# Optimization experiments

Hardware: AMD Instinct MI355X
Metric: run time of the kernel (lower is better)

Reference implementation:

```python
import jax, jax.numpy as jnp
import numpy as np

H = 16  # hidden_size
I = 30  # GRU input_size (hard-coded in module)


def setup_inputs() -> dict:
    key = jax.random.key(0)
    ks = jax.random.split(key, 12)
    B, T = 4096, 512
    s = lambda k, sh: jax.random.normal(k, sh, jnp.float32) * 0.1
    return {
        "x": jax.random.normal(ks[0], (B, T, I), jnp.float32),
        "lengths": jax.random.randint(ks[1], (B,), 1, T + 1),  # valid lengths in [1, T]
        "w_ih": s(ks[2], (3 * H, I)),
        "w_hh": s(ks[3], (3 * H, H)),
        "b_ih": s(ks[4], (3 * H,)),
        "b_hh": s(ks[5], (3 * H,)),
        "fc1_w": s(ks[6], (H, H)), "fc1_b": s(ks[7], (H,)),
        "fc2_w": s(ks[8], (H, H)), "fc2_b": s(ks[9], (H,)),
        "fc3_w": s(ks[10], (H, H)), "fc3_b": s(ks[11], (H,)),
    }


def _gru_last_hidden(x, lengths, w_ih, w_hh, b_ih, b_hh):
    """Run GRU over padded [B,T,I] and return hidden at t = lengths-1 per row.
    Equivalent to pack_padded -> GRU -> pad_packed -> gather output[b, len-1],
    since h_t only depends on steps <= t."""
    B, T, _ = x.shape
    # Precompute input-side gate activations for all steps: [B,T,3H]
    xg = jnp.einsum('bti,gi->btg', x, w_ih) + b_ih
    xr, xz, xn = jnp.split(xg, 3, axis=-1)
    w_hr, w_hz, w_hn = jnp.split(w_hh, 3, axis=0)
    b_hr, b_hz, b_hn = jnp.split(b_hh, 3)
    tidx = lengths - 1  # [B]

    def step(carry, inp):
        h, last = carry
        t, xr_t, xz_t, xn_t = inp
        r = jax.nn.sigmoid(xr_t + h @ w_hr.T + b_hr)
        z = jax.nn.sigmoid(xz_t + h @ w_hz.T + b_hz)
        n = jnp.tanh(xn_t + r * (h @ w_hn.T + b_hn))
        h = (1.0 - z) * n + z * h
        last = jnp.where((tidx == t)[:, None], h, last)  # capture h at final valid step
        return (h, last), None

    h0 = jnp.zeros((B, H), x.dtype)
    (_, last), _ = jax.lax.scan(
        step, (h0, h0),
        (jnp.arange(T),
         xr.transpose(1, 0, 2), xz.transpose(1, 0, 2), xn.transpose(1, 0, 2)))
    return last  # [B,H]


def reference(x, lengths, w_ih, w_hh, b_ih, b_hh,
              fc1_w, fc1_b, fc2_w, fc2_b, fc3_w, fc3_b):
    h = _gru_last_hidden(x, lengths, w_ih, w_hh, b_ih, b_hh)
    e = h @ fc1_w.T + fc1_b
    e = jax.nn.relu(e) @ fc2_w.T + fc2_b   # dropout is identity in eval mode
    e = jax.nn.relu(e) @ fc3_w.T + fc3_b
    return e
```

## Files before the change

kernel.cpp:

```cpp
#include <hip/hip_runtime.h>
#include <cstdint>
#include <cstddef>

typedef float v2f __attribute__((ext_vector_type(2)));

#define HID 16
#define IN  30

#define FAST_RCP(x) __builtin_amdgcn_rcpf(x)

__device__ __forceinline__ float bperm(int baddr, float v) {
    return __int_as_float(__builtin_amdgcn_ds_bpermute(baddr, __float_as_int(v)));
}
__device__ __forceinline__ float dppswap1(float v) {
    return __int_as_float(__builtin_amdgcn_mov_dpp(__float_as_int(v), 0xB1, 0xF, 0xF, true));
}
#define PKFMA(acc, a, b) asm("v_pk_fma_f32 %0, %1, %2, %0" : "+v"(acc) : "v"(a), "v"(b))

typedef __attribute__((address_space(3))) unsigned int       lds_u32_t;
typedef const __attribute__((address_space(1))) unsigned int glb_u32_t;
#define GLOAD_LDS(gp, lp) \
    __builtin_amdgcn_global_load_lds((glb_u32_t*)(gp), (lds_u32_t*)(lp), 4, 0, 0)

__global__ void k_hist(const int* __restrict__ len, int* __restrict__ hist, int B, int T) {
    int i = blockIdx.x * 256 + threadIdx.x;
    if (i < B) atomicAdd(hist + (T - len[i]), 1);
}
__global__ __launch_bounds__(512) void k_scan(const int* __restrict__ hist, int* __restrict__ off) {
    __shared__ int s[512];
    int t = threadIdx.x;
    int v = hist[t];
    s[t] = v; __syncthreads();
    int acc = v;
    for (int o = 1; o < 512; o <<= 1) {
        int add = (t >= o) ? s[t - o] : 0;
        __syncthreads();
        acc += add; s[t] = acc;
        __syncthreads();
    }
    off[t] = acc - v;
}
__global__ void k_scatter(const int* __restrict__ len, int* __restrict__ off,
                          int* __restrict__ perm, int B, int T) {
    int i = blockIdx.x * 256 + threadIdx.x;
    if (i < B) {
        int b = T - len[i];
        int p = atomicAdd(off + b, 1);
        perm[p] = i;
    }
}

__global__ __launch_bounds__(512, 2) void gru_enc_kernel(
    const float* __restrict__ x, const int* __restrict__ lengths,
    const float* __restrict__ w_ih, const float* __restrict__ w_hh,
    const float* __restrict__ b_ih, const float* __restrict__ b_hh,
    const float* __restrict__ fc1w, const float* __restrict__ fc1b,
    const float* __restrict__ fc2w, const float* __restrict__ fc2b,
    const float* __restrict__ fc3w, const float* __restrict__ fc3b,
    float* __restrict__ out, const int* __restrict__ perm,
    int B, int T, int NP, int nblk)
{
    __shared__ __align__(16) float lds[8][4][8][64];

    const int lane = threadIdx.x & 63;
    const int wib  = threadIdx.x >> 6;
    const int rb   = lane & 32;
    const int half = lane & 1;
    const int j    = (lane >> 1) & 15;

    int pos;
    if (wib < 4) pos = 4 * blockIdx.x + wib;
    else         pos = NP - 1 - (4 * blockIdx.x + (wib - 4));
    if (pos < 0 || pos >= NP) return;
    if (wib >= 4 && pos < 4 * nblk) return;

    int ridx = 2 * pos + (rb >> 5);
    if (ridx >= B) ridx = B - 1;
    const int row = perm ? perm[ridx] : ridx;

    const int len = lengths[row];
    const int maxlen = max(len, __shfl_xor(len, 32));

    const float L2E = 1.4426950408889634f;

    const float gsc[3] = { -L2E, -L2E, 2.0f * L2E };

    v2f wih2[3][8];
#pragma unroll
    for (int g = 0; g < 3; ++g) {
        const float* wr = w_ih + (size_t)(g * HID + j) * IN;
#pragma unroll
        for (int m = 0; m < 8; ++m) {
            int p0 = 2 * m, p1 = 2 * m + 1;
            v2f t;
            if (half) { t.x = (p0 == 0) ? 0.0f : wr[14 + p0]; t.y = wr[14 + p1]; }
            else      { t.x = wr[p0]; t.y = (p1 == 15) ? 0.0f : wr[p1]; }
            t.x *= gsc[g]; t.y *= gsc[g];
            wih2[g][m] = t;
        }
    }
    v2f whh2[3][4];
#pragma unroll
    for (int g = 0; g < 3; ++g)
#pragma unroll
        for (int m = 0; m < 4; ++m) {
            const float* wr = w_hh + (size_t)(g * HID + j) * HID + half * 8 + 2 * m;
            v2f t; t.x = wr[0] * gsc[g]; t.y = wr[1] * gsc[g];
            whh2[g][m] = t;
        }

    v2f initR; initR.x = half ? 0.0f : -L2E * (b_ih[j] + b_hh[j]);                 initR.y = 0.0f;
    v2f initZ; initZ.x = half ? 0.0f : -L2E * (b_ih[HID + j] + b_hh[HID + j]);     initZ.y = 0.0f;
    v2f initN; initN.x = half ? 0.0f : 2.0f * L2E * b_ih[2 * HID + j];             initN.y = 0.0f;
    v2f initH; initH.x = half ? 0.0f : 2.0f * L2E * b_hh[2 * HID + j];             initH.y = 0.0f;

    const int kk = min(lane & 31, 29);
    const float* xg = x + (size_t)row * T * IN + kk;

    float* ldsw = &lds[wib][0][0][0];
    const float* ldsr = ldsw + (rb ? 32 : 0) + half * 14;

    int ba0[4], ba1[4];
#pragma unroll
    for (int m = 0; m < 4; ++m) {
        int k0 = half * 8 + 2 * m;
        ba0[m] = (rb | (k0 << 1)) << 2;
        ba1[m] = (rb | ((k0 + 1) << 1)) << 2;
    }

    const int tcap = T - 1;

#define STAGE(cc) do {                                                     \
        const int t0_ = (cc) << 3;                                         \
        float* lb_ = ldsw + (((cc) & 3) << 9);                             \
        _Pragma("unroll")                                                  \
        for (int s_ = 0; s_ < 8; ++s_) {                                   \
            int ts_ = min(t0_ + s_, tcap);                                 \
            GLOAD_LDS(xg + (size_t)ts_ * IN, lb_ + (s_ << 6));             \
        }                                                                  \
    } while (0)

#define STEP(t, cw, s) do {                                                 \
        v2f ar = initR, az = initZ, an = initN, hn = initH;                 \
        v2f xv[8];                                                          \
        _Pragma("unroll")                                                   \
        for (int m_ = 0; m_ < 8; ++m_)                                      \
            xv[m_] = *(const v2f*)((cw) + ((s) << 6) + (m_ << 1));          \
        _Pragma("unroll")                                                   \
        for (int m_ = 0; m_ < 8; ++m_) {                                    \
            PKFMA(ar, wih2[0][m_], xv[m_]);                                 \
            PKFMA(az, wih2[1][m_], xv[m_]);                                 \
            PKFMA(an, wih2[2][m_], xv[m_]);                                 \
        }                                                                   \
        _Pragma("unroll")                                                   \
        for (int m_ = 0; m_ < 4; ++m_) {                                    \
            PKFMA(ar, whh2[0][m_], hb2[m_]);                                \
            PKFMA(az, whh2[1][m_], hb2[m_]);                                \
            PKFMA(hn, whh2[2][m_], hb2[m_]);                                \
        }                                                                   \
        float pr  = ar.x + ar.y;  pr  += dppswap1(pr);                      \
        float pz  = az.x + az.y;  pz  += dppswap1(pz);                      \
        float pxn = an.x + an.y;  pxn += dppswap1(pxn);                     \
        float phn = hn.x + hn.y;  phn += dppswap1(phn);                     \
        float rg = FAST_RCP(1.0f + __builtin_exp2f(pr));                    \
        float zg = FAST_RCP(1.0f + __builtin_exp2f(pz));                    \
        float yy = fmaf(rg, phn, pxn);                                      \
        float ng = fmaf(-2.0f, FAST_RCP(1.0f + __builtin_exp2f(yy)), 1.0f); \
        float hnew = fmaf(zg, h_own - ng, ng);                              \
        last  = ((t) == len - 1) ? hnew : last;                             \
        h_own = hnew;                                                       \
        _Pragma("unroll")                                                   \
        for (int m_ = 0; m_ < 4; ++m_) {                                    \
            hb2[m_].x = bperm(ba0[m_], hnew);                               \
            hb2[m_].y = bperm(ba1[m_], hnew);                               \
        }                                                                   \
    } while (0)

    v2f hb2[4];
#pragma unroll
    for (int m = 0; m < 4; ++m) { hb2[m].x = 0.0f; hb2[m].y = 0.0f; }
    float h_own = 0.0f, last = 0.0f;

    const int nch = (maxlen + 7) >> 3;

    STAGE(0); STAGE(1); STAGE(2);

    for (int c = 0; c < nch; ++c) {
        asm volatile("s_waitcnt vmcnt(16)" ::: "memory");
        STAGE(c + 3);
        const float* cw = ldsr + ((c & 3) << 9);
        const int nst = min(8, maxlen - (c << 3));
        const int tb = c << 3;
#pragma unroll
        for (int s = 0; s < 8; ++s) {
            if (s >= nst) break;
            STEP(tb + s, cw, s);
        }
    }

    float hv[16];
#pragma unroll
    for (int k = 0; k < 16; ++k) hv[k] = __shfl(last, rb + 2 * k, 64);

    float e1 = fc1b[j];
#pragma unroll
    for (int k = 0; k < 16; ++k) e1 = fmaf(fc1w[j * HID + k], hv[k], e1);

    float v1[16];
#pragma unroll
    for (int k = 0; k < 16; ++k) v1[k] = fmaxf(__shfl(e1, rb + 2 * k, 64), 0.0f);

    float e2 = fc2b[j];
#pragma unroll
    for (int k = 0; k < 16; ++k) e2 = fmaf(fc2w[j * HID + k], v1[k], e2);

    float v2a[16];
#pragma unroll
    for (int k = 0; k < 16; ++k) v2a[k] = fmaxf(__shfl(e2, rb + 2 * k, 64), 0.0f);

    float e3 = fc3b[j];
#pragma unroll
    for (int k = 0; k < 16; ++k) e3 = fmaf(fc3w[j * HID + k], v2a[k], e3);

    if (half == 0) out[(size_t)row * HID + j] = e3;
}

extern "C" void kernel_launch(void* const* d_in, const int* in_sizes, int n_in,
                              void* d_out, int out_size, void* d_ws, size_t ws_size,
                              hipStream_t stream) {
    const float* x    = (const float*)d_in[0];
    const int*   lens = (const int*)d_in[1];
    const float* w_ih = (const float*)d_in[2];
    const float* w_hh = (const float*)d_in[3];
    const float* b_ih = (const float*)d_in[4];
    const float* b_hh = (const float*)d_in[5];
    const float* fc1w = (const float*)d_in[6];
    const float* fc1b = (const float*)d_in[7];
    const float* fc2w = (const float*)d_in[8];
    const float* fc2b = (const float*)d_in[9];
    const float* fc3w = (const float*)d_in[10];
    const float* fc3b = (const float*)d_in[11];
    float* out = (float*)d_out;

    const int B = in_sizes[1];
    const int T = (int)(in_sizes[0] / ((size_t)B * IN));

    int* wsI = (int*)d_ws;
    const size_t need = ((size_t)B + 1024) * sizeof(int);
    const bool dosort = (ws_size >= need) && (T <= 512) && (T >= 8);
    int* perm = dosort ? wsI : nullptr;
    int* hist = wsI + B;
    int* off  = wsI + B + 512;

    if (dosort) {
        hipMemsetAsync(hist, 0, 512 * sizeof(int), stream);
        k_hist<<<(B + 255) / 256, 256, 0, stream>>>(lens, hist, B, T);
        k_scan<<<1, 512, 0, stream>>>(hist, off);
        k_scatter<<<(B + 255) / 256, 256, 0, stream>>>(lens, off, perm, B, T);
    }

    const int NP   = (B + 1) / 2;
    const int nblk = (NP + 7) / 8;
    gru_enc_kernel<<<nblk, 512, 0, stream>>>(x, lens, w_ih, w_hh, b_ih, b_hh,
                                             fc1w, fc1b, fc2w, fc2b, fc3w, fc3b,
                                             out, perm, B, T, NP, nblk);
}
```

Baseline: 171.4 us.

## Map one sequence per wavefront with four lanes per hidden unit

Each wavefront now handles one sequence instead of two, and each hidden unit is split across four lanes. Each lane does a quarter of the dot products, and the partial sums are combined with two DPP quad swaps. Per-step LDS staging shrinks, which allows four blocks per CU via launch bounds. Each wave now runs only to its own length rather than the max of a pair, so the `last` capture is dropped. The trade-off is twice as many waves, an extra reduction stage on the serial recurrence, and fewer registers per thread.

```diff
diff --git a/kernel.cpp b/kernel.cpp
--- a/kernel.cpp
+++ b/kernel.cpp
@@ -12,8 +12,11 @@
 __device__ __forceinline__ float bperm(int baddr, float v) {
     return __int_as_float(__builtin_amdgcn_ds_bpermute(baddr, __float_as_int(v)));
 }
-__device__ __forceinline__ float dppswap1(float v) {
+__device__ __forceinline__ float dq1(float v) {
     return __int_as_float(__builtin_amdgcn_mov_dpp(__float_as_int(v), 0xB1, 0xF, 0xF, true));
+}
+__device__ __forceinline__ float dq2(float v) {
+    return __int_as_float(__builtin_amdgcn_mov_dpp(__float_as_int(v), 0x4E, 0xF, 0xF, true));
 }
 #define PKFMA(acc, a, b) asm("v_pk_fma_f32 %0, %1, %2, %0" : "+v"(acc) : "v"(a), "v"(b))
 
@@ -50,7 +53,7 @@
     }
 }
 
-__global__ __launch_bounds__(512, 2) void gru_enc_kernel(
+__global__ __launch_bounds__(512, 4) void gru_enc_kernel(
     const float* __restrict__ x, const int* __restrict__ lengths,
     const float* __restrict__ w_ih, const float* __restrict__ w_hh,
     const float* __restrict__ b_ih, const float* __restrict__ b_hh,
@@ -58,149 +61,133 @@
     const float* __restrict__ fc2w, const float* __restrict__ fc2b,
     const float* __restrict__ fc3w, const float* __restrict__ fc3b,
     float* __restrict__ out, const int* __restrict__ perm,
-    int B, int T, int NP, int nblk)
+    int B, int T, int nblk)
 {
-    __shared__ __align__(16) float lds[8][4][8][64];
+    __shared__ __align__(16) float lds[8][1024];
 
     const int lane = threadIdx.x & 63;
     const int wib  = threadIdx.x >> 6;
-    const int rb   = lane & 32;
-    const int half = lane & 1;
-    const int j    = (lane >> 1) & 15;
+    const int q    = lane & 3;
+    const int j    = lane >> 2;
 
     int pos;
     if (wib < 4) pos = 4 * blockIdx.x + wib;
-    else         pos = NP - 1 - (4 * blockIdx.x + (wib - 4));
-    if (pos < 0 || pos >= NP) return;
+    else         pos = B - 1 - (4 * blockIdx.x + (wib - 4));
+    if (pos < 0 || pos >= B) return;
     if (wib >= 4 && pos < 4 * nblk) return;
 
-    int ridx = 2 * pos + (rb >> 5);
-    if (ridx >= B) ridx = B - 1;
-    const int row = perm ? perm[ridx] : ridx;
-
+    const int row = perm ? perm[pos] : pos;
     const int len = lengths[row];
-    const int maxlen = max(len, __shfl_xor(len, 32));
 
     const float L2E = 1.4426950408889634f;
-
     const float gsc[3] = { -L2E, -L2E, 2.0f * L2E };
 
-    v2f wih2[3][8];
+    v2f wih2[3][4];
 #pragma unroll
     for (int g = 0; g < 3; ++g) {
         const float* wr = w_ih + (size_t)(g * HID + j) * IN;
 #pragma unroll
-        for (int m = 0; m < 8; ++m) {
-            int p0 = 2 * m, p1 = 2 * m + 1;
+        for (int m = 0; m < 4; ++m) {
+            int p0 = q * 8 + 2 * m;
             v2f t;
-            if (half) { t.x = (p0 == 0) ? 0.0f : wr[14 + p0]; t.y = wr[14 + p1]; }
-            else      { t.x = wr[p0]; t.y = (p1 == 15) ? 0.0f : wr[p1]; }
-            t.x *= gsc[g]; t.y *= gsc[g];
+            t.x = (p0     < IN) ? wr[p0]     * gsc[g] : 0.0f;
+            t.y = (p0 + 1 < IN) ? wr[p0 + 1] * gsc[g] : 0.0f;
             wih2[g][m] = t;
         }
     }
-    v2f whh2[3][4];
+    v2f whh2[3][2];
 #pragma unroll
     for (int g = 0; g < 3; ++g)
 #pragma unroll
-        for (int m = 0; m < 4; ++m) {
-            const float* wr = w_hh + (size_t)(g * HID + j) * HID + half * 8 + 2 * m;
+        for (int m = 0; m < 2; ++m) {
+            const float* wr = w_hh + (size_t)(g * HID + j) * HID + q * 4 + 2 * m;
             v2f t; t.x = wr[0] * gsc[g]; t.y = wr[1] * gsc[g];
             whh2[g][m] = t;
         }
 
-    v2f initR; initR.x = half ? 0.0f : -L2E * (b_ih[j] + b_hh[j]);                 initR.y = 0.0f;
-    v2f initZ; initZ.x = half ? 0.0f : -L2E * (b_ih[HID + j] + b_hh[HID + j]);     initZ.y = 0.0f;
-    v2f initN; initN.x = half ? 0.0f : 2.0f * L2E * b_ih[2 * HID + j];             initN.y = 0.0f;
-    v2f initH; initH.x = half ? 0.0f : 2.0f * L2E * b_hh[2 * HID + j];             initH.y = 0.0f;
-
-    const int kk = min(lane & 31, 29);
-    const float* xg = x + (size_t)row * T * IN + kk;
-
-    float* ldsw = &lds[wib][0][0][0];
-    const float* ldsr = ldsw + (rb ? 32 : 0) + half * 14;
-
-    int ba0[4], ba1[4];
-#pragma unroll
-    for (int m = 0; m < 4; ++m) {
-        int k0 = half * 8 + 2 * m;
-        ba0[m] = (rb | (k0 << 1)) << 2;
-        ba1[m] = (rb | ((k0 + 1) << 1)) << 2;
-    }
-
+    v2f initR; initR.x = q ? 0.0f : -L2E * (b_ih[j] + b_hh[j]);               initR.y = 0.0f;
+    v2f initZ; initZ.x = q ? 0.0f : -L2E * (b_ih[HID + j] + b_hh[HID + j]);   initZ.y = 0.0f;
+    v2f initN; initN.x = q ? 0.0f : 2.0f * L2E * b_ih[2 * HID + j];           initN.y = 0.0f;
+    v2f initH; initH.x = q ? 0.0f : 2.0f * L2E * b_hh[2 * HID + j];           initH.y = 0.0f;
+
+    const int word  = min(lane & 31, 29);
+    const int sstep = lane >> 5;
+    const float* xrow = x + (size_t)row * T * IN;
     const int tcap = T - 1;
+
+    float* ldsw = &lds[wib][0];
+    const float* ldsr = ldsw + q * 8;
+
+    int ba[4];
+#pragma unroll
+    for (int m = 0; m < 4; ++m) ba[m] = (16 * q + 4 * m) << 2;
 
 #define STAGE(cc) do {                                                     \
         const int t0_ = (cc) << 3;                                         \
-        float* lb_ = ldsw + (((cc) & 3) << 9);                             \
+        float* lb_ = ldsw + (((cc) & 3) << 8);                             \
         _Pragma("unroll")                                                  \
-        for (int s_ = 0; s_ < 8; ++s_) {                                   \
-            int ts_ = min(t0_ + s_, tcap);                                 \
-            GLOAD_LDS(xg + (size_t)ts_ * IN, lb_ + (s_ << 6));             \
+        for (int i_ = 0; i_ < 4; ++i_) {                                   \
+            int ts_ = min(t0_ + (i_ << 1) + sstep, tcap);                  \
+            GLOAD_LDS(xrow + (size_t)ts_ * IN + word, lb_ + (i_ << 6));    \
         }                                                                  \
     } while (0)
 
-#define STEP(t, cw, s) do {                                                 \
+#define STEP(cw, s) do {                                                    \
+        float4 xa_ = *(const float4*)((cw) + ((s) << 5));                   \
+        float4 xb_ = *(const float4*)((cw) + ((s) << 5) + 4);               \
+        v2f xv[4];                                                          \
+        xv[0].x = xa_.x; xv[0].y = xa_.y; xv[1].x = xa_.z; xv[1].y = xa_.w; \
+        xv[2].x = xb_.x; xv[2].y = xb_.y; xv[3].x = xb_.z; xv[3].y = xb_.w; \
         v2f ar = initR, az = initZ, an = initN, hn = initH;                 \
-        v2f xv[8];                                                          \
         _Pragma("unroll")                                                   \
-        for (int m_ = 0; m_ < 8; ++m_)                                      \
-            xv[m_] = *(const v2f*)((cw) + ((s) << 6) + (m_ << 1));          \
-        _Pragma("unroll")                                                   \
-        for (int m_ = 0; m_ < 8; ++m_) {                                    \
+        for (int m_ = 0; m_ < 4; ++m_) {                                    \
             PKFMA(ar, wih2[0][m_], xv[m_]);                                 \
             PKFMA(az, wih2[1][m_], xv[m_]);                                 \
             PKFMA(an, wih2[2][m_], xv[m_]);                                 \
         }                                                                   \
         _Pragma("unroll")                                                   \
-        for (int m_ = 0; m_ < 4; ++m_) {                                    \
+        for (int m_ = 0; m_ < 2; ++m_) {                                    \
             PKFMA(ar, whh2[0][m_], hb2[m_]);                                \
             PKFMA(az, whh2[1][m_], hb2[m_]);                                \
             PKFMA(hn, whh2[2][m_], hb2[m_]);                                \
         }                                                                   \
-        float pr  = ar.x + ar.y;  pr  += dppswap1(pr);                      \
-        float pz  = az.x + az.y;  pz  += dppswap1(pz);                      \
-        float pxn = an.x + an.y;  pxn += dppswap1(pxn);                     \
-        float phn = hn.x + hn.y;  phn += dppswap1(phn);                     \
+        float pr  = ar.x + ar.y;  pr  += dq1(pr);  pr  += dq2(pr);          \
+        float pz  = az.x + az.y;  pz  += dq1(pz);  pz  += dq2(pz);          \
+        float pxn = an.x + an.y;  pxn += dq1(pxn); pxn += dq2(pxn);         \
+        float phn = hn.x + hn.y;  phn += dq1(phn); phn += dq2(phn);         \
         float rg = FAST_RCP(1.0f + __builtin_exp2f(pr));                    \
         float zg = FAST_RCP(1.0f + __builtin_exp2f(pz));                    \
         float yy = fmaf(rg, phn, pxn);                                      \
         float ng = fmaf(-2.0f, FAST_RCP(1.0f + __builtin_exp2f(yy)), 1.0f); \
-        float hnew = fmaf(zg, h_own - ng, ng);                              \
-        last  = ((t) == len - 1) ? hnew : last;                             \
-        h_own = hnew;                                                       \
-        _Pragma("unroll")                                                   \
-        for (int m_ = 0; m_ < 4; ++m_) {                                    \
-            hb2[m_].x = bperm(ba0[m_], hnew);                               \
-            hb2[m_].y = bperm(ba1[m_], hnew);                               \
-        }                                                                   \
+        h_own = fmaf(zg, h_own - ng, ng);                                   \
+        float b0 = bperm(ba[0], h_own), b1 = bperm(ba[1], h_own);           \
+        float b2 = bperm(ba[2], h_own), b3 = bperm(ba[3], h_own);           \
+        hb2[0].x = b0; hb2[0].y = b1; hb2[1].x = b2; hb2[1].y = b3;         \
     } while (0)
 
-    v2f hb2[4];
-#pragma unroll
-    for (int m = 0; m < 4; ++m) { hb2[m].x = 0.0f; hb2[m].y = 0.0f; }
-    float h_own = 0.0f, last = 0.0f;
-
-    const int nch = (maxlen + 7) >> 3;
+    v2f hb2[2];
+    hb2[0].x = 0.0f; hb2[0].y = 0.0f; hb2[1].x = 0.0f; hb2[1].y = 0.0f;
+    float h_own = 0.0f;
+
+    const int nch = (len + 7) >> 3;
 
     STAGE(0); STAGE(1); STAGE(2);
 
     for (int c = 0; c < nch; ++c) {
-        asm volatile("s_waitcnt vmcnt(16)" ::: "memory");
+        asm volatile("s_waitcnt vmcnt(8)" ::: "memory");
         STAGE(c + 3);
-        const float* cw = ldsr + ((c & 3) << 9);
-        const int nst = min(8, maxlen - (c << 3));
-        const int tb = c << 3;
+        const float* cw = ldsr + ((c & 3) << 8);
+        const int nst = min(8, len - (c << 3));
 #pragma unroll
         for (int s = 0; s < 8; ++s) {
             if (s >= nst) break;
-            STEP(tb + s, cw, s);
+            STEP(cw, s);
         }
     }
 
     float hv[16];
 #pragma unroll
-    for (int k = 0; k < 16; ++k) hv[k] = __shfl(last, rb + 2 * k, 64);
+    for (int k = 0; k < 16; ++k) hv[k] = __shfl(h_own, 4 * k, 64);
 
     float e1 = fc1b[j];
 #pragma unroll
@@ -208,7 +195,7 @@
 
     float v1[16];
 #pragma unroll
-    for (int k = 0; k < 16; ++k) v1[k] = fmaxf(__shfl(e1, rb + 2 * k, 64), 0.0f);
+    for (int k = 0; k < 16; ++k) v1[k] = fmaxf(__shfl(e1, 4 * k, 64), 0.0f);
 
     float e2 = fc2b[j];
 #pragma unroll
@@ -216,13 +203,13 @@
 
     float v2a[16];
 #pragma unroll
-    for (int k = 0; k < 16; ++k) v2a[k] = fmaxf(__shfl(e2, rb + 2 * k, 64), 0.0f);
+    for (int k = 0; k < 16; ++k) v2a[k] = fmaxf(__shfl(e2, 4 * k, 64), 0.0f);
 
     float e3 = fc3b[j];
 #pragma unroll
     for (int k = 0; k < 16; ++k) e3 = fmaf(fc3w[j * HID + k], v2a[k], e3);
 
-    if (half == 0) out[(size_t)row * HID + j] = e3;
+    if (q == 0) out[(size_t)row * HID + j] = e3;
 }
 
 extern "C" void kernel_launch(void* const* d_in, const int* in_sizes, int n_in,
@@ -259,9 +246,8 @@
         k_scatter<<<(B + 255) / 256, 256, 0, stream>>>(lens, off, perm, B, T);
     }
 
-    const int NP   = (B + 1) / 2;
-    const int nblk = (NP + 7) / 8;
+    const int nblk = (B + 7) / 8;
     gru_enc_kernel<<<nblk, 512, 0, stream>>>(x, lens, w_ih, w_hh, b_ih, b_hh,
                                              fc1w, fc1b, fc2w, fc2b, fc3w, fc3b,
-                                             out, perm, B, T, NP, nblk);
-}
+                                             out, perm, B, T, nblk);
+}
```

Result: faster. 167.5 us (-2.3%).
